# Kernel tuning notes

Measured on AMD Instinct MI355X. Metric: run time of the kernel, lower is better.

The kernel has to match this reference:

```python
import jax, jax.numpy as jnp
import numpy as np

U_NUM, I_NUM, EMBED, NUM_LAYERS = 100000, 50000, 64, 3
N_NODES = U_NUM + I_NUM
BATCH = 8192


def _build_laplacian(rng):
    # Faithful to buildLaplacianMat: symmetric bipartite rating matrix with
    # D^-1/2 A D^-1/2 normalization (degree = count of nonzeros per row).
    nnz = 2_000_000
    u = rng.integers(0, U_NUM, nnz)
    i = rng.integers(0, I_NUM, nnz)
    lin = np.unique(u.astype(np.int64) * I_NUM + i)  # dedupe (user,item) pairs
    u = (lin // I_NUM).astype(np.int32)
    i = (lin % I_NUM).astype(np.int32)
    rating = rng.integers(1, 6, u.shape[0]).astype(np.float32)
    rows = np.concatenate([u, i + U_NUM])
    cols = np.concatenate([i + U_NUM, u])
    vals = np.concatenate([rating, rating])
    deg = np.bincount(rows, minlength=N_NODES)
    dinv = np.where(deg > 0, deg.astype(np.float64) ** -0.5, 0.0).astype(np.float32)
    vals = dinv[rows] * vals * dinv[cols]
    return rows, cols, vals


def setup_inputs() -> dict:
    key = jax.random.key(0)
    k1, k2 = jax.random.split(key)
    rng = np.random.default_rng(0)
    rows, cols, vals = _build_laplacian(rng)
    # xavier_uniform over [num, embed]: bound = sqrt(6/(fan_in+fan_out))
    bu = float(np.sqrt(6.0 / (U_NUM + EMBED)))
    bi = float(np.sqrt(6.0 / (I_NUM + EMBED)))
    uEmbd = jax.random.uniform(k1, (U_NUM, EMBED), jnp.float32, -bu, bu)
    iEmbd = jax.random.uniform(k2, (I_NUM, EMBED), jnp.float32, -bi, bi)
    userIdx = jnp.asarray(rng.integers(0, U_NUM, BATCH), dtype=jnp.int64)
    itemIdx = jnp.asarray(rng.integers(0, I_NUM, BATCH), dtype=jnp.int64)
    return {
        "uEmbd": uEmbd,
        "iEmbd": iEmbd,
        "lap_rows": jnp.asarray(rows, jnp.int32),
        "lap_cols": jnp.asarray(cols, jnp.int32),
        "lap_vals": jnp.asarray(vals, jnp.float32),
        "userIdx": userIdx,
        "itemIdx": itemIdx,
    }


def _spmm(rows, cols, vals, x):
    # sparse [N,N] @ dense [N,D] via edge-list gather + segment-sum
    return jax.ops.segment_sum(vals[:, None] * x[cols], rows, num_segments=N_NODES)


def reference(uEmbd, iEmbd, lap_rows, lap_cols, lap_vals, userIdx, itemIdx):
    feats = jnp.concatenate([uEmbd, iEmbd], axis=0)  # [N, D]
    acc = feats
    f = feats
    for _ in range(NUM_LAYERS):
        f = _spmm(lap_rows, lap_cols, lap_vals, f)
        acc = acc + f
    final = acc / (NUM_LAYERS + 1)  # mean over stacked layer embeddings
    ue = final[userIdx]                      # [B, D]
    ie = final[itemIdx + U_NUM]              # [B, D]
    return jnp.sum(ue * ie, axis=1)          # [B]
```

## Files before the change

### kernel.cpp

```cpp
#include <hip/hip_runtime.h>

#define U_NUMC 100000
#define I_NUMC 50000
#define NNODES 150000
#define EMB 64
#define NBATCH 8192
#define NB_I ((I_NUMC + 255) / 256)

__global__ __launch_bounds__(256) void k_zero(int* __restrict__ p, int n) {
    int i = blockIdx.x * blockDim.x + threadIdx.x;
    if (i < n) p[i] = 0;
}

__global__ __launch_bounds__(256) void k_uptr(const int* __restrict__ rows1, int E1,
                                              int* __restrict__ uptr) {
    int r = blockIdx.x * blockDim.x + threadIdx.x;
    if (r > U_NUMC) return;
    int lo = 0, hi = E1;
    while (lo < hi) {
        int mid = (lo + hi) >> 1;
        if (rows1[mid] < r) lo = mid + 1; else hi = mid;
    }
    uptr[r] = lo;
}

__global__ __launch_bounds__(256) void k_hist(const int* __restrict__ cols1, int E1,
                                              int* __restrict__ hist) {
    int e = blockIdx.x * blockDim.x + threadIdx.x;
    if (e >= E1) return;
    atomicAdd(&hist[cols1[e] - U_NUMC], 1);
}

__global__ __launch_bounds__(256) void k_scan1(const int* __restrict__ hist,
                                               int* __restrict__ bsum) {
    int b = blockIdx.x, t = threadIdx.x;
    int idx = b * 256 + t;
    int v = (idx < I_NUMC) ? hist[idx] : 0;
    #pragma unroll
    for (int o = 32; o; o >>= 1) v += __shfl_xor(v, o);
    __shared__ int ws4[4];
    if ((t & 63) == 0) ws4[t >> 6] = v;
    __syncthreads();
    if (t == 0) bsum[b] = ws4[0] + ws4[1] + ws4[2] + ws4[3];
}

__global__ __launch_bounds__(256) void k_scan2(const int* __restrict__ bsum,
                                               int* __restrict__ boff,
                                               int* __restrict__ iptr) {
    __shared__ int lds[256];
    int t = threadIdx.x;
    int v = (t < NB_I) ? bsum[t] : 0;
    int x = v;
    #pragma unroll
    for (int o = 1; o < 256; o <<= 1) {
        lds[t] = x; __syncthreads();
        int y = (t >= o) ? lds[t - o] : 0; __syncthreads();
        x += y;
    }
    if (t < NB_I) boff[t] = x - v;
    if (t == 255) iptr[I_NUMC] = x;
}

__global__ __launch_bounds__(256) void k_scan3(const int* __restrict__ hist,
                                               const int* __restrict__ boff,
                                               int* __restrict__ iptr,
                                               int* __restrict__ cursor) {
    __shared__ int lds[256];
    int b = blockIdx.x, t = threadIdx.x;
    int idx = b * 256 + t;
    int v = (idx < I_NUMC) ? hist[idx] : 0;
    int x = v;
    #pragma unroll
    for (int o = 1; o < 256; o <<= 1) {
        lds[t] = x; __syncthreads();
        int y = (t >= o) ? lds[t - o] : 0; __syncthreads();
        x += y;
    }
    if (idx < I_NUMC) {
        int excl = boff[b] + x - v;
        iptr[idx] = excl;
        cursor[idx] = excl;
    }
}

__global__ __launch_bounds__(256) void k_scatter(const int* __restrict__ rows1,
                                                 const int* __restrict__ cols1,
                                                 const float* __restrict__ vals1,
                                                 int E1,
                                                 int* __restrict__ cursor,
                                                 int2* __restrict__ item_uv) {
    int e = blockIdx.x * blockDim.x + threadIdx.x;
    if (e >= E1) return;
    int i = cols1[e] - U_NUMC;
    int pos = atomicAdd(&cursor[i], 1);
    item_uv[pos] = make_int2(rows1[e], __float_as_int(vals1[e]));
}

template <int FIRST, int LAST>
__global__ __launch_bounds__(256) void k_spmm(const float* __restrict__ uE,
                                              const float* __restrict__ iE,
                                              const float* __restrict__ f,
                                              float* __restrict__ fn,
                                              float* __restrict__ acc,
                                              const int* __restrict__ uptr,
                                              const int* __restrict__ cols1,
                                              const float* __restrict__ vals1,
                                              const int* __restrict__ iptr,
                                              const int2* __restrict__ item_uv) {
    int wave = (blockIdx.x * blockDim.x + threadIdx.x) >> 6;
    int lane = threadIdx.x & 63;
    if (wave >= NNODES) return;

    const bool isUser = (wave < U_NUMC);
    int beg, end;
    if (isUser) { beg = uptr[wave];           end = uptr[wave + 1]; }
    else        { int i = wave - U_NUMC; beg = iptr[i]; end = iptr[i + 1]; }

    const float* fb;
    if (FIRST) fb = isUser ? (iE - (size_t)U_NUMC * EMB) : uE;
    else       fb = f;

    float sum = 0.f;
    for (int base = beg; base < end; base += 64) {
        int idx = base + lane;
        int ld = min(idx, end - 1);
        int c; float v;
        if (isUser) {
            c = cols1[ld];
            v = (idx < end) ? vals1[ld] : 0.f;
        } else {
            int2 e = item_uv[ld];
            c = e.x;
            v = (idx < end) ? __int_as_float(e.y) : 0.f;
        }
        int n = min(64, end - base);
        for (int j = 0; j < n; j += 8) {
            float l[8], vv[8];
            #pragma unroll
            for (int t = 0; t < 8; ++t) {
                int cj = __shfl(c, j + t);
                vv[t] = __shfl(v, j + t);
                l[t] = fb[(size_t)cj * EMB + lane];
            }
            #pragma unroll
            for (int t = 0; t < 8; ++t) sum += vv[t] * l[t];
        }
    }
    int o = wave * EMB + lane;
    if (!LAST) fn[o] = sum;
    if (FIRST) {
        float own = isUser ? uE[(size_t)wave * EMB + lane]
                           : iE[(size_t)(wave - U_NUMC) * EMB + lane];
        acc[o] = own + sum;
    } else {
        acc[o] += sum;
    }
}

__global__ __launch_bounds__(256) void k_out(const float* __restrict__ acc,
                                             const int* __restrict__ userIdx,
                                             const int* __restrict__ itemIdx,
                                             float* __restrict__ out) {
    int wave = (blockIdx.x * blockDim.x + threadIdx.x) >> 6;
    int lane = threadIdx.x & 63;
    if (wave >= NBATCH) return;
    int u = userIdx[wave];
    int it = itemIdx[wave] + U_NUMC;
    float p = acc[u * EMB + lane] * acc[it * EMB + lane];
    #pragma unroll
    for (int offd = 32; offd; offd >>= 1) p += __shfl_xor(p, offd);
    if (lane == 0) out[wave] = p * (1.0f / 16.0f);
}

extern "C" void kernel_launch(void* const* d_in, const int* in_sizes, int n_in,
                              void* d_out, int out_size, void* d_ws, size_t ws_size,
                              hipStream_t stream) {
    const float* uE      = (const float*)d_in[0];
    const float* iE      = (const float*)d_in[1];
    const int*   rows    = (const int*)d_in[2];
    const int*   cols    = (const int*)d_in[3];
    const float* vals    = (const float*)d_in[4];
    const int*   userIdx = (const int*)d_in[5];
    const int*   itemIdx = (const int*)d_in[6];
    const int E  = in_sizes[2];
    const int E1 = E / 2;

    char* ws = (char*)d_ws;
    size_t off = 0;
    auto alloc = [&](size_t bytes) -> void* {
        off = (off + 255) & ~(size_t)255;
        void* p = ws + off;
        off += bytes;
        return p;
    };
    float* f0      = (float*)alloc((size_t)NNODES * EMB * 4);
    float* f1      = (float*)alloc((size_t)NNODES * EMB * 4);
    float* acc     = (float*)alloc((size_t)NNODES * EMB * 4);
    int*   uptr    = (int*)alloc((size_t)(U_NUMC + 1) * 4);
    int*   iptr    = (int*)alloc((size_t)(I_NUMC + 1) * 4);
    int*   hist    = (int*)alloc((size_t)I_NUMC * 4);
    int*   cursor  = (int*)alloc((size_t)I_NUMC * 4);
    int*   bsum    = (int*)alloc((size_t)NB_I * 4);
    int*   boff    = (int*)alloc((size_t)NB_I * 4);
    int2*  item_uv = (int2*)alloc((size_t)E1 * 8);

    k_zero<<<(I_NUMC + 255) / 256, 256, 0, stream>>>(hist, I_NUMC);
    k_uptr<<<(U_NUMC + 256) / 256, 256, 0, stream>>>(rows, E1, uptr);
    k_hist<<<(E1 + 255) / 256, 256, 0, stream>>>(cols, E1, hist);
    k_scan1<<<NB_I, 256, 0, stream>>>(hist, bsum);
    k_scan2<<<1, 256, 0, stream>>>(bsum, boff, iptr);
    k_scan3<<<NB_I, 256, 0, stream>>>(hist, boff, iptr, cursor);
    k_scatter<<<(E1 + 255) / 256, 256, 0, stream>>>(rows, cols, vals, E1,
                                                    cursor, item_uv);

    const int spmm_blocks = NNODES / 4;
    k_spmm<1, 0><<<spmm_blocks, 256, 0, stream>>>(uE, iE, nullptr, f1, acc,
                                                  uptr, cols, vals, iptr, item_uv);
    k_spmm<0, 0><<<spmm_blocks, 256, 0, stream>>>(uE, iE, f1, f0, acc,
                                                  uptr, cols, vals, iptr, item_uv);
    k_spmm<0, 1><<<spmm_blocks, 256, 0, stream>>>(uE, iE, f0, nullptr, acc,
                                                  uptr, cols, vals, iptr, item_uv);

    k_out<<<NBATCH / 4, 256, 0, stream>>>(acc, userIdx, itemIdx, (float*)d_out);
}
```

Before: 735.0 us.

## Replace per-item atomic scatter with two-level bucket scatter plus LDS local sort

The CSC transpose build now scatters edges into buckets of 16 items using one global atomic counter per bucket, with the sub-item index packed into the high bits of the user id. A new per-bucket kernel stages each bucket in shared memory and places every edge into its final item slot using shared-memory atomics. The goal is to cut contention on global atomics and make the scatter writes more local, at the cost of one extra kernel and an extra pass over the edge array. The bit packing assumes user ids fit in 17 bits.

Measured after the change: 778.6 us. +5.9%, slower.

```diff
diff --git a/kernel.cpp b/kernel.cpp
--- a/kernel.cpp
+++ b/kernel.cpp
@@ -6,6 +6,9 @@
 #define EMB 64
 #define NBATCH 8192
 #define NB_I ((I_NUMC + 255) / 256)
+#define BSH 4
+#define NBKT ((I_NUMC + 15) >> BSH)
+#define BCAP 2048
 
 __global__ __launch_bounds__(256) void k_zero(int* __restrict__ p, int n) {
     int i = blockIdx.x * blockDim.x + threadIdx.x;
@@ -64,7 +67,7 @@
 __global__ __launch_bounds__(256) void k_scan3(const int* __restrict__ hist,
                                                const int* __restrict__ boff,
                                                int* __restrict__ iptr,
-                                               int* __restrict__ cursor) {
+                                               int* __restrict__ bcur) {
     __shared__ int lds[256];
     int b = blockIdx.x, t = threadIdx.x;
     int idx = b * 256 + t;
@@ -79,7 +82,7 @@
     if (idx < I_NUMC) {
         int excl = boff[b] + x - v;
         iptr[idx] = excl;
-        cursor[idx] = excl;
+        if ((idx & ((1 << BSH) - 1)) == 0) bcur[idx >> BSH] = excl;
     }
 }
 
@@ -87,13 +90,41 @@
                                                  const int* __restrict__ cols1,
                                                  const float* __restrict__ vals1,
                                                  int E1,
-                                                 int* __restrict__ cursor,
+                                                 int* __restrict__ bcur,
                                                  int2* __restrict__ item_uv) {
     int e = blockIdx.x * blockDim.x + threadIdx.x;
     if (e >= E1) return;
     int i = cols1[e] - U_NUMC;
-    int pos = atomicAdd(&cursor[i], 1);
-    item_uv[pos] = make_int2(rows1[e], __float_as_int(vals1[e]));
+    int pos = atomicAdd(&bcur[i >> BSH], 1);
+    item_uv[pos] = make_int2(((i & ((1 << BSH) - 1)) << 17) | rows1[e],
+                             __float_as_int(vals1[e]));
+}
+
+__global__ __launch_bounds__(256) void k_bsort(const int* __restrict__ iptr,
+                                               int2* __restrict__ item_uv) {
+    __shared__ int2 st[BCAP];
+    __shared__ int lcur[1 << BSH];
+    int b = blockIdx.x, t = threadIdx.x;
+    int ibase = b << BSH;
+    if (t < (1 << BSH)) {
+        int item = ibase + t;
+        lcur[t] = (item < I_NUMC) ? iptr[item] : 0;
+    }
+    int iend = ibase + (1 << BSH); if (iend > I_NUMC) iend = I_NUMC;
+    int wbeg = iptr[ibase];
+    int wend = iptr[iend];
+    __syncthreads();
+    for (int off = wbeg; off < wend; off += BCAP) {
+        int n = min(BCAP, wend - off);
+        for (int k = t; k < n; k += 256) st[k] = item_uv[off + k];
+        __syncthreads();
+        for (int k = t; k < n; k += 256) {
+            int2 e = st[k];
+            int pos = atomicAdd(&lcur[e.x >> 17], 1);
+            item_uv[pos] = make_int2(e.x & 0x1FFFF, e.y);
+        }
+        __syncthreads();
+    }
 }
 
 template <int FIRST, int LAST>
@@ -199,7 +230,7 @@
     int*   uptr    = (int*)alloc((size_t)(U_NUMC + 1) * 4);
     int*   iptr    = (int*)alloc((size_t)(I_NUMC + 1) * 4);
     int*   hist    = (int*)alloc((size_t)I_NUMC * 4);
-    int*   cursor  = (int*)alloc((size_t)I_NUMC * 4);
+    int*   bcur    = (int*)alloc((size_t)NBKT * 4);
     int*   bsum    = (int*)alloc((size_t)NB_I * 4);
     int*   boff    = (int*)alloc((size_t)NB_I * 4);
     int2*  item_uv = (int2*)alloc((size_t)E1 * 8);
@@ -209,9 +240,10 @@
     k_hist<<<(E1 + 255) / 256, 256, 0, stream>>>(cols, E1, hist);
     k_scan1<<<NB_I, 256, 0, stream>>>(hist, bsum);
     k_scan2<<<1, 256, 0, stream>>>(bsum, boff, iptr);
-    k_scan3<<<NB_I, 256, 0, stream>>>(hist, boff, iptr, cursor);
+    k_scan3<<<NB_I, 256, 0, stream>>>(hist, boff, iptr, bcur);
     k_scatter<<<(E1 + 255) / 256, 256, 0, stream>>>(rows, cols, vals, E1,
-                                                    cursor, item_uv);
+                                                    bcur, item_uv);
+    k_bsort<<<NBKT, 256, 0, stream>>>(iptr, item_uv);
 
     const int spmm_blocks = NNODES / 4;
     k_spmm<1, 0><<<spmm_blocks, 256, 0, stream>>>(uE, iE, nullptr, f1, acc,
```

## Drop accumulator traffic, use scalar-uniform edge loads, partition scatter atomics

Applied to the files above, without the earlier changes.

Each SpMM layer now writes only its own output buffer, with no read-modify-write of a full-size accumulator. The final scoring kernel sums the layer outputs for just the 8192 batch rows. The SpMM inner loop reads edge indices and values as wave-uniform loads through readfirstlane instead of shuffles, and uses eight independent partial sums to allow more memory-level parallelism. The scatter kernel splits items into eight classes by block so atomics on the same cursor group stay together. The trade-off is that the scatter reads the column array eight times over, and summation order changes slightly.

Result: faster. 677.4 us (-7.8%).

```diff
diff --git a/kernel.cpp b/kernel.cpp
--- a/kernel.cpp
+++ b/kernel.cpp
@@ -89,19 +89,40 @@
                                                  int E1,
                                                  int* __restrict__ cursor,
                                                  int2* __restrict__ item_uv) {
-    int e = blockIdx.x * blockDim.x + threadIdx.x;
-    if (e >= E1) return;
-    int i = cols1[e] - U_NUMC;
-    int pos = atomicAdd(&cursor[i], 1);
-    item_uv[pos] = make_int2(rows1[e], __float_as_int(vals1[e]));
-}
-
-template <int FIRST, int LAST>
+    const int cls  = blockIdx.x & 7;
+    const int bsub = blockIdx.x >> 3;
+    const int nb   = gridDim.x >> 3;
+    const int E4   = E1 >> 2;
+    const int4* c4p = (const int4*)cols1;
+    for (int q = bsub * 256 + threadIdx.x; q < E4; q += nb * 256) {
+        int4 c4 = c4p[q];
+        #pragma unroll
+        for (int t = 0; t < 4; ++t) {
+            int cv = (t == 0) ? c4.x : (t == 1) ? c4.y : (t == 2) ? c4.z : c4.w;
+            int i = cv - U_NUMC;
+            if (((i >> 3) & 7) != cls) continue;
+            int e = q * 4 + t;
+            int pos = atomicAdd(&cursor[i], 1);
+            item_uv[pos] = make_int2(rows1[e], __float_as_int(vals1[e]));
+        }
+    }
+    if (bsub == 0) {
+        int e = E4 * 4 + threadIdx.x;
+        if (e < E1) {
+            int i = cols1[e] - U_NUMC;
+            if (((i >> 3) & 7) == cls) {
+                int pos = atomicAdd(&cursor[i], 1);
+                item_uv[pos] = make_int2(rows1[e], __float_as_int(vals1[e]));
+            }
+        }
+    }
+}
+
+template <int FIRST>
 __global__ __launch_bounds__(256) void k_spmm(const float* __restrict__ uE,
                                               const float* __restrict__ iE,
                                               const float* __restrict__ f,
                                               float* __restrict__ fn,
-                                              float* __restrict__ acc,
                                               const int* __restrict__ uptr,
                                               const int* __restrict__ cols1,
                                               const float* __restrict__ vals1,
@@ -115,60 +136,73 @@
     int beg, end;
     if (isUser) { beg = uptr[wave];           end = uptr[wave + 1]; }
     else        { int i = wave - U_NUMC; beg = iptr[i]; end = iptr[i + 1]; }
+    beg = __builtin_amdgcn_readfirstlane(beg);
+    end = __builtin_amdgcn_readfirstlane(end);
 
     const float* fb;
     if (FIRST) fb = isUser ? (iE - (size_t)U_NUMC * EMB) : uE;
     else       fb = f;
 
-    float sum = 0.f;
-    for (int base = beg; base < end; base += 64) {
-        int idx = base + lane;
-        int ld = min(idx, end - 1);
-        int c; float v;
-        if (isUser) {
-            c = cols1[ld];
-            v = (idx < end) ? vals1[ld] : 0.f;
-        } else {
-            int2 e = item_uv[ld];
-            c = e.x;
-            v = (idx < end) ? __int_as_float(e.y) : 0.f;
-        }
-        int n = min(64, end - base);
-        for (int j = 0; j < n; j += 8) {
-            float l[8], vv[8];
+    float s0 = 0.f, s1 = 0.f, s2 = 0.f, s3 = 0.f;
+    float s4 = 0.f, s5 = 0.f, s6 = 0.f, s7 = 0.f;
+    int j = beg;
+    if (isUser) {
+        for (; j + 8 <= end; j += 8) {
             #pragma unroll
             for (int t = 0; t < 8; ++t) {
-                int cj = __shfl(c, j + t);
-                vv[t] = __shfl(v, j + t);
-                l[t] = fb[(size_t)cj * EMB + lane];
+                int   c = cols1[j + t];
+                float v = vals1[j + t];
+                float l = fb[(size_t)c * EMB + lane];
+                if (t == 0) s0 += v * l; else if (t == 1) s1 += v * l;
+                else if (t == 2) s2 += v * l; else if (t == 3) s3 += v * l;
+                else if (t == 4) s4 += v * l; else if (t == 5) s5 += v * l;
+                else if (t == 6) s6 += v * l; else s7 += v * l;
             }
+        }
+        for (; j < end; ++j)
+            s0 += vals1[j] * fb[(size_t)cols1[j] * EMB + lane];
+    } else {
+        for (; j + 8 <= end; j += 8) {
             #pragma unroll
-            for (int t = 0; t < 8; ++t) sum += vv[t] * l[t];
-        }
-    }
-    int o = wave * EMB + lane;
-    if (!LAST) fn[o] = sum;
-    if (FIRST) {
-        float own = isUser ? uE[(size_t)wave * EMB + lane]
-                           : iE[(size_t)(wave - U_NUMC) * EMB + lane];
-        acc[o] = own + sum;
-    } else {
-        acc[o] += sum;
-    }
-}
-
-__global__ __launch_bounds__(256) void k_out(const float* __restrict__ acc,
+            for (int t = 0; t < 8; ++t) {
+                int2 e = item_uv[j + t];
+                float v = __int_as_float(e.y);
+                float l = fb[(size_t)e.x * EMB + lane];
+                if (t == 0) s0 += v * l; else if (t == 1) s1 += v * l;
+                else if (t == 2) s2 += v * l; else if (t == 3) s3 += v * l;
+                else if (t == 4) s4 += v * l; else if (t == 5) s5 += v * l;
+                else if (t == 6) s6 += v * l; else s7 += v * l;
+            }
+        }
+        for (; j < end; ++j) {
+            int2 e = item_uv[j];
+            s0 += __int_as_float(e.y) * fb[(size_t)e.x * EMB + lane];
+        }
+    }
+    float sum = ((s0 + s1) + (s2 + s3)) + ((s4 + s5) + (s6 + s7));
+    fn[(size_t)wave * EMB + lane] = sum;
+}
+
+__global__ __launch_bounds__(256) void k_out(const float* __restrict__ uE,
+                                             const float* __restrict__ iE,
+                                             const float* __restrict__ g1,
+                                             const float* __restrict__ g2,
+                                             const float* __restrict__ g3,
                                              const int* __restrict__ userIdx,
                                              const int* __restrict__ itemIdx,
                                              float* __restrict__ out) {
     int wave = (blockIdx.x * blockDim.x + threadIdx.x) >> 6;
     int lane = threadIdx.x & 63;
     if (wave >= NBATCH) return;
-    int u = userIdx[wave];
-    int it = itemIdx[wave] + U_NUMC;
-    float p = acc[u * EMB + lane] * acc[it * EMB + lane];
-    #pragma unroll
-    for (int offd = 32; offd; offd >>= 1) p += __shfl_xor(p, offd);
+    int u  = userIdx[wave];
+    int it = itemIdx[wave];
+    size_t ou = (size_t)u * EMB + lane;
+    size_t oi = (size_t)(U_NUMC + it) * EMB + lane;
+    float a = uE[ou] + g1[ou] + g2[ou] + g3[ou];
+    float b = iE[(size_t)it * EMB + lane] + g1[oi] + g2[oi] + g3[oi];
+    float p = a * b;
+    #pragma unroll
+    for (int o = 32; o; o >>= 1) p += __shfl_xor(p, o);
     if (lane == 0) out[wave] = p * (1.0f / 16.0f);
 }
 
@@ -193,9 +227,9 @@
         off += bytes;
         return p;
     };
-    float* f0      = (float*)alloc((size_t)NNODES * EMB * 4);
-    float* f1      = (float*)alloc((size_t)NNODES * EMB * 4);
-    float* acc     = (float*)alloc((size_t)NNODES * EMB * 4);
+    float* g1      = (float*)alloc((size_t)NNODES * EMB * 4);
+    float* g2      = (float*)alloc((size_t)NNODES * EMB * 4);
+    float* g3      = (float*)alloc((size_t)NNODES * EMB * 4);
     int*   uptr    = (int*)alloc((size_t)(U_NUMC + 1) * 4);
     int*   iptr    = (int*)alloc((size_t)(I_NUMC + 1) * 4);
     int*   hist    = (int*)alloc((size_t)I_NUMC * 4);
@@ -210,16 +244,16 @@
     k_scan1<<<NB_I, 256, 0, stream>>>(hist, bsum);
     k_scan2<<<1, 256, 0, stream>>>(bsum, boff, iptr);
     k_scan3<<<NB_I, 256, 0, stream>>>(hist, boff, iptr, cursor);
-    k_scatter<<<(E1 + 255) / 256, 256, 0, stream>>>(rows, cols, vals, E1,
-                                                    cursor, item_uv);
+    k_scatter<<<2048, 256, 0, stream>>>(rows, cols, vals, E1, cursor, item_uv);
 
     const int spmm_blocks = NNODES / 4;
-    k_spmm<1, 0><<<spmm_blocks, 256, 0, stream>>>(uE, iE, nullptr, f1, acc,
-                                                  uptr, cols, vals, iptr, item_uv);
-    k_spmm<0, 0><<<spmm_blocks, 256, 0, stream>>>(uE, iE, f1, f0, acc,
-                                                  uptr, cols, vals, iptr, item_uv);
-    k_spmm<0, 1><<<spmm_blocks, 256, 0, stream>>>(uE, iE, f0, nullptr, acc,
-                                                  uptr, cols, vals, iptr, item_uv);
-
-    k_out<<<NBATCH / 4, 256, 0, stream>>>(acc, userIdx, itemIdx, (float*)d_out);
-}
+    k_spmm<1><<<spmm_blocks, 256, 0, stream>>>(uE, iE, nullptr, g1,
+                                               uptr, cols, vals, iptr, item_uv);
+    k_spmm<0><<<spmm_blocks, 256, 0, stream>>>(uE, iE, g1, g2,
+                                               uptr, cols, vals, iptr, item_uv);
+    k_spmm<0><<<spmm_blocks, 256, 0, stream>>>(uE, iE, g2, g3,
+                                               uptr, cols, vals, iptr, item_uv);
+
+    k_out<<<NBATCH / 4, 256, 0, stream>>>(uE, iE, g1, g2, g3,
+                                          userIdx, itemIdx, (float*)d_out);
+}
```
